# Optimization experiments

Hardware: AMD Instinct MI355X
Metric: run time of the kernel (lower is better)

The kernel has to match this reference:

```python
import jax, jax.numpy as jnp
import numpy as np

DX = 0.1
DY = 0.1
W_B = 1000.0
W_PARALLEL = 1000.0
W_DIV = 100.0
EPS = 1e-10


def setup_inputs() -> dict:
    key = jax.random.key(0)
    k1, k2 = jax.random.split(key)
    outputs = jax.random.normal(k1, (2, 3, 256, 256, 64), dtype=jnp.float32)
    targets = jax.random.normal(k2, (2, 4, 256, 256, 64), dtype=jnp.float32)
    return {"outputs": outputs, "targets": targets}


def _corners(f):
    # 8 shifted views f[..., i:, j:, k:] (with 0 -> [0:-1], 1 -> [1:]) on dims 2,3,4
    s0, s1 = slice(0, -1), slice(1, None)
    return {(i, j, k): f[:, :, (s1 if i else s0), (s1 if j else s0), (s1 if k else s0)]
            for i in (0, 1) for j in (0, 1) for k in (0, 1)}


def _forward(outputs, targets):
    bx_p, by_p, bz_p = outputs[:, 0:1], outputs[:, 1:2], outputs[:, 2:3]
    bx_t, by_t, bz_t = targets[:, 0:1], targets[:, 1:2], targets[:, 2:3]

    loss_b = (jnp.mean((bx_p**2 + by_p**2 - bx_t**2 - by_t**2) ** 2 / (bx_t**2 + by_t**2 + EPS))
              + jnp.mean((bz_p - bz_t) ** 4 / (bz_t**2 + EPS)))
    loss_parallel = jnp.mean((bx_p * by_t - by_p * bx_t) ** 2
                             / (bx_t**2 + by_t**2 + bz_t**2 + EPS))

    bx = _corners(bx_p)
    by = _corners(by_p)
    bz = _corners(bz_p)
    z = _corners(targets[:, 3:4])

    num = (0.25 * (bx[1, 0, 0] + bx[1, 1, 0] + bx[1, 0, 1] + bx[1, 1, 1]) * DY * 0.5 * (z[1, 0, 1] - z[1, 0, 0] + z[1, 1, 1] - z[1, 1, 0])
           - 0.25 * (bx[0, 0, 0] + bx[0, 1, 0] + bx[0, 0, 1] + bx[0, 1, 1]) * DY * 0.5 * (z[0, 0, 1] - z[0, 0, 0] + z[0, 1, 1] - z[0, 1, 0])
           + 0.25 * (by[0, 1, 0] + by[1, 1, 0] + by[0, 1, 1] + by[1, 1, 1]) * DX * 0.5 * (z[0, 1, 1] - z[0, 1, 0] + z[1, 1, 1] - z[1, 1, 0])
           - 0.25 * (by[0, 0, 0] + by[1, 0, 0] + by[0, 0, 1] + by[1, 0, 1]) * DX * 0.5 * (z[0, 0, 1] - z[0, 0, 0] + z[1, 0, 1] - z[1, 0, 0])
           + 0.25 * (bz[0, 0, 1] + bz[0, 1, 1] + bz[1, 0, 1] + bz[1, 1, 1]) * DX * DY
           - 0.25 * (bz[0, 0, 0] + bz[0, 1, 0] + bz[1, 0, 0] + bz[1, 1, 0]) * DX * DY
           + (bx[0, 0, 1] + bx[1, 0, 1] + bx[1, 1, 1]) * DY * (z[0, 0, 1] - z[1, 0, 1]) / 6
           + (bx[0, 1, 1] + bx[1, 1, 1] + bx[1, 0, 1]) * DY * (z[0, 1, 1] - z[1, 1, 1]) / 6
           + (by[1, 0, 1] + by[1, 1, 1] + by[0, 1, 1]) * DX * (z[1, 0, 1] - z[1, 1, 1]) / 6
           + (by[0, 0, 1] + by[0, 1, 1] + by[1, 1, 1]) * DX * (z[0, 0, 1] - z[0, 1, 1]) / 6
           - (bx[0, 0, 0] + bx[1, 0, 0] + bx[1, 1, 0]) * DY * (z[0, 0, 0] - z[1, 0, 0]) / 6
           - (bx[0, 1, 0] + bx[1, 1, 0] + bx[1, 0, 0]) * DY * (z[0, 1, 0] - z[1, 1, 0]) / 6
           - (by[1, 0, 0] + by[1, 1, 0] + by[0, 1, 0]) * DX * (z[1, 0, 0] - z[1, 1, 0]) / 6
           - (by[0, 0, 0] + by[0, 1, 0] + by[1, 1, 0]) * DX * (z[0, 0, 0] - z[0, 1, 0]) / 6)

    bx_c = sum(bx[c] for c in sorted(bx)) * 0.125
    by_c = sum(by[c] for c in sorted(by)) * 0.125
    bz_c = sum(bz[c] for c in sorted(bz)) * 0.125
    den = bx_c**2 + by_c**2 + bz_c**2 + EPS

    loss_div = jnp.mean(num**2 / den) / DX**2 / DY**2

    return (W_B * loss_b + W_PARALLEL * loss_parallel, W_DIV * loss_div)


def reference(outputs, targets):
    return _forward(outputs, targets)
```

## Files before the change

kernel.cpp:

```cpp
#include <hip/hip_runtime.h>
#include <stdint.h>

constexpr int B = 2, X = 256, Y = 256, Z = 64;
constexpr int CO = X * Y * Z;
constexpr int YZ = Y * Z;
constexpr long long N_PTS   = (long long)B * X * Y * Z;
constexpr long long M_CELLS = (long long)B * (X-1) * (Y-1) * (Z-1);

constexpr int RPB = 16;
constexpr int TPB = 256;
constexpr int WPB = TPB / 64;
constexpr int BLOCKS = B * (Y / RPB) * X;

#define EPSc 1e-10f
#define SIXTH (1.0f / 6.0f)
#define RCPF(v) __builtin_amdgcn_rcpf(v)

typedef float fvec4 __attribute__((ext_vector_type(4)));

#define F4C(v, c) (((c) == 0) ? (v).x : ((c) == 1) ? (v).y : ((c) == 2) ? (v).z : (v).w)
#define LD4(p)  (*(const fvec4*)(p))
#define LDNT(p) __builtin_nontemporal_load((const fvec4*)(p))

__global__ __launch_bounds__(TPB, 4) void loss_main(const float* __restrict__ outs,
                                                    const float* __restrict__ tgts,
                                                    double* __restrict__ partial) {
    const int lane = threadIdx.x & 63;
    const int wv   = threadIdx.x >> 6;

    const int bid = (int)blockIdx.x;
    const int blk = (bid & 7) * (BLOCKS / 8) + (bid >> 3);

    const int b  = blk >> 12;
    const int r  = blk & 4095;
    const int sy = r >> 8;
    const int x  = r & 255;

    const int row_l = wv * 4 + (lane >> 4);
    const int zi    = (lane & 15) << 2;
    const int y     = sy * RPB + row_l;

    const int xp = (x < X - 1) ? (x + 1) : x;
    const int yp = (y < Y - 1) ? (y + 1) : y;
    const bool xvalid = (x < X - 1);
    const bool yvalid = (y < Y - 1);

    const float* ob = outs + (size_t)b * 3 * CO;
    const float* tb = tgts + (size_t)b * 4 * CO;

    const size_t o00 = (size_t)x  * YZ + (size_t)y  * Z + zi;
    const size_t o01 = (size_t)x  * YZ + (size_t)yp * Z + zi;
    const size_t o10 = (size_t)xp * YZ + (size_t)y  * Z + zi;
    const size_t o11 = (size_t)xp * YZ + (size_t)yp * Z + zi;

    const fvec4 bx00v = LD4(ob + 0 * CO + o00);
    const fvec4 by00v = LD4(ob + 1 * CO + o00);
    const fvec4 bz00v = LD4(ob + 2 * CO + o00);
    const fvec4 zc00v = LD4(tb + 3 * CO + o00);
    const fvec4 bx01v = LD4(ob + 0 * CO + o01);
    const fvec4 by01v = LD4(ob + 1 * CO + o01);
    const fvec4 bz01v = LD4(ob + 2 * CO + o01);
    const fvec4 zc01v = LD4(tb + 3 * CO + o01);
    const fvec4 bx10v = LD4(ob + 0 * CO + o10);
    const fvec4 by10v = LD4(ob + 1 * CO + o10);
    const fvec4 bz10v = LD4(ob + 2 * CO + o10);
    const fvec4 zc10v = LD4(tb + 3 * CO + o10);
    const fvec4 bx11v = LD4(ob + 0 * CO + o11);
    const fvec4 by11v = LD4(ob + 1 * CO + o11);
    const fvec4 bz11v = LD4(ob + 2 * CO + o11);
    const fvec4 zc11v = LD4(tb + 3 * CO + o11);
    const fvec4 t0 = LDNT(tb + 0 * CO + o00);
    const fvec4 t1 = LDNT(tb + 1 * CO + o00);
    const fvec4 t2 = LDNT(tb + 2 * CO + o00);

    double s_pt = 0.0, s_dv = 0.0;

    {
        float pt4 = 0.0f;
        #pragma unroll
        for (int c = 0; c < 4; ++c) {
            const float bxp = F4C(bx00v, c), byp = F4C(by00v, c), bzp = F4C(bz00v, c);
            const float bxt = F4C(t0, c), byt = F4C(t1, c), bzt = F4C(t2, c);
            const float bxt2 = bxt * bxt, byt2 = byt * byt, bzt2 = bzt * bzt;
            const float dxy = bxt2 + byt2;
            const float tq = bxp * bxp + byp * byp - dxy;
            const float e1 = tq * tq * RCPF(dxy + EPSc);
            const float dd = bzp - bzt;
            const float dd2 = dd * dd;
            const float e2 = dd2 * dd2 * RCPF(bzt2 + EPSc);
            const float cr = bxp * byt - byp * bxt;
            const float e3 = cr * cr * RCPF(dxy + bzt2 + EPSc);
            pt4 += e1 + e2 + e3;
        }
        s_pt += (double)pt4;
    }

    if (xvalid) {
        float sxp[5], sxm[5], syp[5], sym[5];
        float zxp[5], zxm[5], zyp[5], zym[5];
        float Sx[5], Sy[5], Sz[5], G2[5];

        #pragma unroll
        for (int t = 0; t < 4; ++t) {
            const float bx00 = F4C(bx00v, t), bx10 = F4C(bx10v, t);
            const float bx01 = F4C(bx01v, t), bx11 = F4C(bx11v, t);
            const float by00 = F4C(by00v, t), by10 = F4C(by10v, t);
            const float by01 = F4C(by01v, t), by11 = F4C(by11v, t);
            const float bz00 = F4C(bz00v, t), bz10 = F4C(bz10v, t);
            const float bz01 = F4C(bz01v, t), bz11 = F4C(bz11v, t);
            const float zc00 = F4C(zc00v, t), zc10 = F4C(zc10v, t);
            const float zc01 = F4C(zc01v, t), zc11 = F4C(zc11v, t);

            sxp[t] = bx10 + bx11;   sxm[t] = bx00 + bx01;
            syp[t] = by01 + by11;   sym[t] = by00 + by10;
            zxp[t] = zc10 + zc11;   zxm[t] = zc00 + zc01;
            zyp[t] = zc01 + zc11;   zym[t] = zc00 + zc10;
            Sx[t] = sxp[t] + sxm[t];
            Sy[t] = syp[t] + sym[t];
            Sz[t] = (bz00 + bz01) + (bz10 + bz11);
            G2[t] = 0.025f * Sz[t]
                  + SIXTH * ((bx00 + sxp[t]) * (zc00 - zc10)
                           + (bx01 + sxp[t]) * (zc01 - zc11)
                           + (by10 + syp[t]) * (zc10 - zc11)
                           + (by00 + syp[t]) * (zc00 - zc01));
        }
        sxp[4] = __shfl_down(sxp[0], 1);
        sxm[4] = __shfl_down(sxm[0], 1);
        syp[4] = __shfl_down(syp[0], 1);
        sym[4] = __shfl_down(sym[0], 1);
        zxp[4] = __shfl_down(zxp[0], 1);
        zxm[4] = __shfl_down(zxm[0], 1);
        zyp[4] = __shfl_down(zyp[0], 1);
        zym[4] = __shfl_down(zym[0], 1);
        Sz[4]  = __shfl_down(Sz[0],  1);
        G2[4]  = __shfl_down(G2[0],  1);
        Sx[4] = sxp[4] + sxm[4];
        Sy[4] = syp[4] + sym[4];

        float dv4 = 0.0f;
        #pragma unroll
        for (int c = 0; c < 4; ++c) {
            const float fx = (sxp[c] + sxp[c+1]) * (zxp[c+1] - zxp[c])
                           - (sxm[c] + sxm[c+1]) * (zxm[c+1] - zxm[c])
                           + (syp[c] + syp[c+1]) * (zyp[c+1] - zyp[c])
                           - (sym[c] + sym[c+1]) * (zym[c+1] - zym[c]);
            const float num2 = 0.125f * fx + (G2[c+1] - G2[c]);
            const float SxS = Sx[c] + Sx[c+1];
            const float SyS = Sy[c] + Sy[c+1];
            const float SzS = Sz[c] + Sz[c+1];
            const float q = SxS * SxS + SyS * SyS + SzS * SzS;
            const float den = 0.015625f * q + EPSc;
            const float v = num2 * num2 * RCPF(den);
            const bool ok = yvalid && ((zi + c) < Z - 1);
            dv4 += ok ? v : 0.0f;
        }
        s_dv += (double)dv4;
    }

    for (int off = 32; off > 0; off >>= 1) {
        s_pt += __shfl_down(s_pt, off);
        s_dv += __shfl_down(s_dv, off);
    }

    __shared__ double lds_pt[WPB];
    __shared__ double lds_dv[WPB];
    if (lane == 0) { lds_pt[wv] = s_pt; lds_dv[wv] = s_dv; }
    __syncthreads();
    if (threadIdx.x == 0) {
        double p = 0.0, d = 0.0;
        #pragma unroll
        for (int w = 0; w < WPB; ++w) { p += lds_pt[w]; d += lds_dv[w]; }
        partial[2 * blk]     = p;
        partial[2 * blk + 1] = d;
    }
}

__global__ __launch_bounds__(256) void loss_finalize(const double* __restrict__ partial,
                                                     float* __restrict__ out) {
    double s0 = 0.0, s1 = 0.0;
    for (int i = threadIdx.x; i < BLOCKS; i += 256) {
        s0 += partial[2 * i];
        s1 += partial[2 * i + 1];
    }
    const int lane = threadIdx.x & 63;
    const int wave = threadIdx.x >> 6;
    for (int off = 32; off > 0; off >>= 1) {
        s0 += __shfl_down(s0, off);
        s1 += __shfl_down(s1, off);
    }
    __shared__ double l0[4], l1[4];
    if (lane == 0) { l0[wave] = s0; l1[wave] = s1; }
    __syncthreads();
    if (threadIdx.x == 0) {
        double p = 0.0, d = 0.0;
        #pragma unroll
        for (int w = 0; w < 4; ++w) { p += l0[w]; d += l1[w]; }
        const double out0 = 1000.0 * (p / (double)N_PTS);
        const double out1 = 10000.0 * (d / (double)M_CELLS);
        out[0] = (float)out0;
        out[1] = (float)out1;
    }
}

extern "C" void kernel_launch(void* const* d_in, const int* in_sizes, int n_in,
                              void* d_out, int out_size, void* d_ws, size_t ws_size,
                              hipStream_t stream) {
    const float* outs = (const float*)d_in[0];
    const float* tgts = (const float*)d_in[1];
    float* out = (float*)d_out;
    double* partial = (double*)d_ws;

    loss_main<<<BLOCKS, TPB, 0, stream>>>(outs, tgts, partial);
    loss_finalize<<<1, 256, 0, stream>>>(partial, out);
}
```

Baseline: 269.1 us.

## Process four x-planes per block with rolling register reuse and prefetch

Each block now walks XS=4 consecutive x-planes instead of one, keeping the loaded y/y+1 stencil rows of the previous plane in a 3-slot register ring so each plane is loaded once rather than twice. Loads for the next plane are issued before computing the current one to overlap memory with math, and offsets use 32-bit arithmetic. This cuts redundant global reads of the x+1 neighbour plane and per-block overhead, at the cost of more registers (launch bounds lowered to 2 waves/SIMD hint) and fewer blocks.

After: 250.2 us. 1.08x faster.

```diff
diff --git a/kernel.cpp b/kernel.cpp
--- a/kernel.cpp
+++ b/kernel.cpp
@@ -8,9 +8,10 @@
 constexpr long long M_CELLS = (long long)B * (X-1) * (Y-1) * (Z-1);
 
 constexpr int RPB = 16;
+constexpr int XS  = 4;
 constexpr int TPB = 256;
 constexpr int WPB = TPB / 64;
-constexpr int BLOCKS = B * (Y / RPB) * X;
+constexpr int BLOCKS = B * (Y / RPB) * (X / XS);
 
 #define EPSc 1e-10f
 #define SIXTH (1.0f / 6.0f)
@@ -19,10 +20,10 @@
 typedef float fvec4 __attribute__((ext_vector_type(4)));
 
 #define F4C(v, c) (((c) == 0) ? (v).x : ((c) == 1) ? (v).y : ((c) == 2) ? (v).z : (v).w)
-#define LD4(p)  (*(const fvec4*)(p))
-#define LDNT(p) __builtin_nontemporal_load((const fvec4*)(p))
-
-__global__ __launch_bounds__(TPB, 4) void loss_main(const float* __restrict__ outs,
+#define LD4(base, off)  (*(const fvec4*)((base) + (off)))
+#define LDNT(base, off) __builtin_nontemporal_load((const fvec4*)((base) + (off)))
+
+__global__ __launch_bounds__(TPB, 2) void loss_main(const float* __restrict__ outs,
                                                     const float* __restrict__ tgts,
                                                     double* __restrict__ partial) {
     const int lane = threadIdx.x & 63;
@@ -31,130 +32,139 @@
     const int bid = (int)blockIdx.x;
     const int blk = (bid & 7) * (BLOCKS / 8) + (bid >> 3);
 
-    const int b  = blk >> 12;
-    const int r  = blk & 4095;
-    const int sy = r >> 8;
-    const int x  = r & 255;
+    const int b  = blk >> 10;
+    const int r  = blk & 1023;
+    const int sy = r >> 6;
+    const int xc = r & 63;
+    const int x0 = xc * XS;
 
     const int row_l = wv * 4 + (lane >> 4);
     const int zi    = (lane & 15) << 2;
     const int y     = sy * RPB + row_l;
-
-    const int xp = (x < X - 1) ? (x + 1) : x;
-    const int yp = (y < Y - 1) ? (y + 1) : y;
-    const bool xvalid = (x < X - 1);
+    const int yp    = (y < Y - 1) ? (y + 1) : y;
     const bool yvalid = (y < Y - 1);
 
     const float* ob = outs + (size_t)b * 3 * CO;
     const float* tb = tgts + (size_t)b * 4 * CO;
 
-    const size_t o00 = (size_t)x  * YZ + (size_t)y  * Z + zi;
-    const size_t o01 = (size_t)x  * YZ + (size_t)yp * Z + zi;
-    const size_t o10 = (size_t)xp * YZ + (size_t)y  * Z + zi;
-    const size_t o11 = (size_t)xp * YZ + (size_t)yp * Z + zi;
-
-    const fvec4 bx00v = LD4(ob + 0 * CO + o00);
-    const fvec4 by00v = LD4(ob + 1 * CO + o00);
-    const fvec4 bz00v = LD4(ob + 2 * CO + o00);
-    const fvec4 zc00v = LD4(tb + 3 * CO + o00);
-    const fvec4 bx01v = LD4(ob + 0 * CO + o01);
-    const fvec4 by01v = LD4(ob + 1 * CO + o01);
-    const fvec4 bz01v = LD4(ob + 2 * CO + o01);
-    const fvec4 zc01v = LD4(tb + 3 * CO + o01);
-    const fvec4 bx10v = LD4(ob + 0 * CO + o10);
-    const fvec4 by10v = LD4(ob + 1 * CO + o10);
-    const fvec4 bz10v = LD4(ob + 2 * CO + o10);
-    const fvec4 zc10v = LD4(tb + 3 * CO + o10);
-    const fvec4 bx11v = LD4(ob + 0 * CO + o11);
-    const fvec4 by11v = LD4(ob + 1 * CO + o11);
-    const fvec4 bz11v = LD4(ob + 2 * CO + o11);
-    const fvec4 zc11v = LD4(tb + 3 * CO + o11);
-    const fvec4 t0 = LDNT(tb + 0 * CO + o00);
-    const fvec4 t1 = LDNT(tb + 1 * CO + o00);
-    const fvec4 t2 = LDNT(tb + 2 * CO + o00);
+    const uint32_t yZzi  = (uint32_t)y  * Z + zi;
+    const uint32_t ypZzi = (uint32_t)yp * Z + zi;
+    constexpr uint32_t C1 = (uint32_t)CO, C2 = 2u * CO, C3 = 3u * CO;
+
+    fvec4 sbx0[3], sby0[3], sbz0[3], szc0[3];
+    fvec4 sbx1[3], sby1[3], sbz1[3], szc1[3];
+    fvec4 tg0[2], tg1[2], tg2[2];
+
+    auto issue_stn = [&](int c, int s) {
+        const uint32_t xb = (uint32_t)((x0 + c < X) ? (x0 + c) : (X - 1)) * YZ;
+        const uint32_t o0 = xb + yZzi, o1 = xb + ypZzi;
+        sbx0[s] = LD4(ob, o0);        sbx1[s] = LD4(ob, o1);
+        sby0[s] = LD4(ob, C1 + o0);   sby1[s] = LD4(ob, C1 + o1);
+        sbz0[s] = LD4(ob, C2 + o0);   sbz1[s] = LD4(ob, C2 + o1);
+        szc0[s] = LD4(tb, C3 + o0);   szc1[s] = LD4(tb, C3 + o1);
+    };
+    auto issue_tgt = [&](int c, int s) {
+        const uint32_t o0 = (uint32_t)(x0 + c) * YZ + yZzi;
+        tg0[s] = LDNT(tb, o0);
+        tg1[s] = LDNT(tb, C1 + o0);
+        tg2[s] = LDNT(tb, C2 + o0);
+    };
+
+    issue_stn(0, 0);
+    issue_tgt(0, 0);
 
     double s_pt = 0.0, s_dv = 0.0;
 
-    {
-        float pt4 = 0.0f;
-        #pragma unroll
-        for (int c = 0; c < 4; ++c) {
-            const float bxp = F4C(bx00v, c), byp = F4C(by00v, c), bzp = F4C(bz00v, c);
-            const float bxt = F4C(t0, c), byt = F4C(t1, c), bzt = F4C(t2, c);
-            const float bxt2 = bxt * bxt, byt2 = byt * byt, bzt2 = bzt * bzt;
-            const float dxy = bxt2 + byt2;
-            const float tq = bxp * bxp + byp * byp - dxy;
-            const float e1 = tq * tq * RCPF(dxy + EPSc);
-            const float dd = bzp - bzt;
-            const float dd2 = dd * dd;
-            const float e2 = dd2 * dd2 * RCPF(bzt2 + EPSc);
-            const float cr = bxp * byt - byp * bxt;
-            const float e3 = cr * cr * RCPF(dxy + bzt2 + EPSc);
-            pt4 += e1 + e2 + e3;
+    #pragma unroll
+    for (int i = 0; i <= XS; ++i) {
+        const int cs = i % 3;
+        const int ps = (i + 2) % 3;
+        const int ts = i & 1;
+
+        if (i < XS)      issue_stn(i + 1, (i + 1) % 3);
+        if (i < XS - 1)  issue_tgt(i + 1, (i + 1) & 1);
+
+        if (i < XS) {
+            float pt4 = 0.0f;
+            #pragma unroll
+            for (int c = 0; c < 4; ++c) {
+                const float bxp = F4C(sbx0[cs], c), byp = F4C(sby0[cs], c), bzp = F4C(sbz0[cs], c);
+                const float bxt = F4C(tg0[ts], c), byt = F4C(tg1[ts], c), bzt = F4C(tg2[ts], c);
+                const float bxt2 = bxt * bxt, byt2 = byt * byt, bzt2 = bzt * bzt;
+                const float dxy = bxt2 + byt2;
+                const float tq = bxp * bxp + byp * byp - dxy;
+                const float e1 = tq * tq * RCPF(dxy + EPSc);
+                const float dd = bzp - bzt;
+                const float dd2 = dd * dd;
+                const float e2 = dd2 * dd2 * RCPF(bzt2 + EPSc);
+                const float cr = bxp * byt - byp * bxt;
+                const float e3 = cr * cr * RCPF(dxy + bzt2 + EPSc);
+                pt4 += e1 + e2 + e3;
+            }
+            s_pt += (double)pt4;
         }
-        s_pt += (double)pt4;
-    }
-
-    if (xvalid) {
-        float sxp[5], sxm[5], syp[5], sym[5];
-        float zxp[5], zxm[5], zyp[5], zym[5];
-        float Sx[5], Sy[5], Sz[5], G2[5];
-
-        #pragma unroll
-        for (int t = 0; t < 4; ++t) {
-            const float bx00 = F4C(bx00v, t), bx10 = F4C(bx10v, t);
-            const float bx01 = F4C(bx01v, t), bx11 = F4C(bx11v, t);
-            const float by00 = F4C(by00v, t), by10 = F4C(by10v, t);
-            const float by01 = F4C(by01v, t), by11 = F4C(by11v, t);
-            const float bz00 = F4C(bz00v, t), bz10 = F4C(bz10v, t);
-            const float bz01 = F4C(bz01v, t), bz11 = F4C(bz11v, t);
-            const float zc00 = F4C(zc00v, t), zc10 = F4C(zc10v, t);
-            const float zc01 = F4C(zc01v, t), zc11 = F4C(zc11v, t);
-
-            sxp[t] = bx10 + bx11;   sxm[t] = bx00 + bx01;
-            syp[t] = by01 + by11;   sym[t] = by00 + by10;
-            zxp[t] = zc10 + zc11;   zxm[t] = zc00 + zc01;
-            zyp[t] = zc01 + zc11;   zym[t] = zc00 + zc10;
-            Sx[t] = sxp[t] + sxm[t];
-            Sy[t] = syp[t] + sym[t];
-            Sz[t] = (bz00 + bz01) + (bz10 + bz11);
-            G2[t] = 0.025f * Sz[t]
-                  + SIXTH * ((bx00 + sxp[t]) * (zc00 - zc10)
-                           + (bx01 + sxp[t]) * (zc01 - zc11)
-                           + (by10 + syp[t]) * (zc10 - zc11)
-                           + (by00 + syp[t]) * (zc00 - zc01));
+
+        if (i >= 1 && (x0 + i - 1) < X - 1) {
+            float sxp[5], sxm[5], syp[5], sym[5];
+            float zxp[5], zxm[5], zyp[5], zym[5];
+            float Sx[5], Sy[5], Sz[5], G2[5];
+
+            #pragma unroll
+            for (int t = 0; t < 4; ++t) {
+                const float bx00 = F4C(sbx0[ps], t), bx10 = F4C(sbx0[cs], t);
+                const float bx01 = F4C(sbx1[ps], t), bx11 = F4C(sbx1[cs], t);
+                const float by00 = F4C(sby0[ps], t), by10 = F4C(sby0[cs], t);
+                const float by01 = F4C(sby1[ps], t), by11 = F4C(sby1[cs], t);
+                const float bz00 = F4C(sbz0[ps], t), bz10 = F4C(sbz0[cs], t);
+                const float bz01 = F4C(sbz1[ps], t), bz11 = F4C(sbz1[cs], t);
+                const float zc00 = F4C(szc0[ps], t), zc10 = F4C(szc0[cs], t);
+                const float zc01 = F4C(szc1[ps], t), zc11 = F4C(szc1[cs], t);
+
+                sxp[t] = bx10 + bx11;   sxm[t] = bx00 + bx01;
+                syp[t] = by01 + by11;   sym[t] = by00 + by10;
+                zxp[t] = zc10 + zc11;   zxm[t] = zc00 + zc01;
+                zyp[t] = zc01 + zc11;   zym[t] = zc00 + zc10;
+                Sx[t] = sxp[t] + sxm[t];
+                Sy[t] = syp[t] + sym[t];
+                Sz[t] = (bz00 + bz01) + (bz10 + bz11);
+                G2[t] = 0.025f * Sz[t]
+                      + SIXTH * ((bx00 + sxp[t]) * (zc00 - zc10)
+                               + (bx01 + sxp[t]) * (zc01 - zc11)
+                               + (by10 + syp[t]) * (zc10 - zc11)
+                               + (by00 + syp[t]) * (zc00 - zc01));
+            }
+            sxp[4] = __shfl_down(sxp[0], 1);
+            sxm[4] = __shfl_down(sxm[0], 1);
+            syp[4] = __shfl_down(syp[0], 1);
+            sym[4] = __shfl_down(sym[0], 1);
+            zxp[4] = __shfl_down(zxp[0], 1);
+            zxm[4] = __shfl_down(zxm[0], 1);
+            zyp[4] = __shfl_down(zyp[0], 1);
+            zym[4] = __shfl_down(zym[0], 1);
+            Sz[4]  = __shfl_down(Sz[0],  1);
+            G2[4]  = __shfl_down(G2[0],  1);
+            Sx[4] = sxp[4] + sxm[4];
+            Sy[4] = syp[4] + sym[4];
+
+            float dv4 = 0.0f;
+            #pragma unroll
+            for (int c = 0; c < 4; ++c) {
+                const float fx = (sxp[c] + sxp[c+1]) * (zxp[c+1] - zxp[c])
+                               - (sxm[c] + sxm[c+1]) * (zxm[c+1] - zxm[c])
+                               + (syp[c] + syp[c+1]) * (zyp[c+1] - zyp[c])
+                               - (sym[c] + sym[c+1]) * (zym[c+1] - zym[c]);
+                const float num2 = 0.125f * fx + (G2[c+1] - G2[c]);
+                const float SxS = Sx[c] + Sx[c+1];
+                const float SyS = Sy[c] + Sy[c+1];
+                const float SzS = Sz[c] + Sz[c+1];
+                const float q = SxS * SxS + SyS * SyS + SzS * SzS;
+                const float den = 0.015625f * q + EPSc;
+                const float v = num2 * num2 * RCPF(den);
+                const bool ok = yvalid && ((zi + c) < Z - 1);
+                dv4 += ok ? v : 0.0f;
+            }
+            s_dv += (double)dv4;
         }
-        sxp[4] = __shfl_down(sxp[0], 1);
-        sxm[4] = __shfl_down(sxm[0], 1);
-        syp[4] = __shfl_down(syp[0], 1);
-        sym[4] = __shfl_down(sym[0], 1);
-        zxp[4] = __shfl_down(zxp[0], 1);
-        zxm[4] = __shfl_down(zxm[0], 1);
-        zyp[4] = __shfl_down(zyp[0], 1);
-        zym[4] = __shfl_down(zym[0], 1);
-        Sz[4]  = __shfl_down(Sz[0],  1);
-        G2[4]  = __shfl_down(G2[0],  1);
-        Sx[4] = sxp[4] + sxm[4];
-        Sy[4] = syp[4] + sym[4];
-
-        float dv4 = 0.0f;
-        #pragma unroll
-        for (int c = 0; c < 4; ++c) {
-            const float fx = (sxp[c] + sxp[c+1]) * (zxp[c+1] - zxp[c])
-                           - (sxm[c] + sxm[c+1]) * (zxm[c+1] - zxm[c])
-                           + (syp[c] + syp[c+1]) * (zyp[c+1] - zyp[c])
-                           - (sym[c] + sym[c+1]) * (zym[c+1] - zym[c]);
-            const float num2 = 0.125f * fx + (G2[c+1] - G2[c]);
-            const float SxS = Sx[c] + Sx[c+1];
-            const float SyS = Sy[c] + Sy[c+1];
-            const float SzS = Sz[c] + Sz[c+1];
-            const float q = SxS * SxS + SyS * SyS + SzS * SzS;
-            const float den = 0.015625f * q + EPSc;
-            const float v = num2 * num2 * RCPF(den);
-            const bool ok = yvalid && ((zi + c) < Z - 1);
-            dv4 += ok ? v : 0.0f;
-        }
-        s_dv += (double)dv4;
     }
 
     for (int off = 32; off > 0; off >>= 1) {
```
